# Optimization experiments

Hardware: AMD Instinct MI355X
Metric: run time of the kernel (lower is better)

## Reference

```python
import jax, jax.numpy as jnp
import numpy as np

N_NODES = 50000
N_EDGES = 800000
NFEAT = 256
NHID = 128
NCLASS = 40
NLAYERS = 3


def setup_inputs() -> dict:
    key = jax.random.key(0)
    ks = jax.random.split(key, 8)
    x = jax.random.normal(ks[0], (N_NODES, NFEAT), dtype=jnp.float32)
    edge_src = jax.random.randint(ks[1], (N_EDGES,), 0, N_NODES, dtype=jnp.int32)
    edge_dst = jax.random.randint(ks[2], (N_EDGES,), 0, N_NODES, dtype=jnp.int32)
    # Kaiming-ish scaled params
    W_in = jax.random.normal(ks[3], (NFEAT, NHID), dtype=jnp.float32) / np.sqrt(NFEAT)
    b_in = jnp.zeros((NHID,), dtype=jnp.float32)
    W_mlps = jax.random.normal(ks[4], (NLAYERS, NHID, NHID), dtype=jnp.float32) / np.sqrt(NHID)
    b_mlps = jnp.zeros((NLAYERS, NHID), dtype=jnp.float32)
    W_out = jax.random.normal(ks[5], (NHID, NCLASS), dtype=jnp.float32) / np.sqrt(NHID)
    b_out = jnp.zeros((NCLASS,), dtype=jnp.float32)
    return {"x": x, "edge_src": edge_src, "edge_dst": edge_dst,
            "W_in": W_in, "b_in": b_in, "W_mlps": W_mlps, "b_mlps": b_mlps,
            "W_out": W_out, "b_out": b_out}


def reference(x, edge_src, edge_dst, W_in, b_in, W_mlps, b_mlps, W_out, b_out):
    # Dropout is identity in eval mode (training=False).
    n = x.shape[0]
    h = jax.nn.relu(x @ W_in + b_in)                       # [N, H]
    for i in range(NLAYERS):
        # GINConv with eps=0: h' = h + sum_{(s->d) in E} h[s] scattered to d
        agg = jax.ops.segment_sum(h[edge_src], edge_dst, num_segments=n)
        h = jax.nn.relu((h + agg) @ W_mlps[i] + b_mlps[i])  # [N, H]
    logits = h @ W_out + b_out                              # [N, C]
    return jax.nn.log_softmax(logits, axis=1)
```

## Files before the change

kernel.cpp:

```cpp
#include <hip/hip_runtime.h>
#include <math.h>

#define NHID 128
#define NFEAT 256
#define NCLASS 40

typedef __bf16 bf16x8 __attribute__((ext_vector_type(8)));
typedef __bf16 bf16x4 __attribute__((ext_vector_type(4)));
typedef float floatx4 __attribute__((ext_vector_type(4)));


__global__ __launch_bounds__(256) void bucket_hist(const int* __restrict__ edst,
                                                   int* __restrict__ bucket_counts,
                                                   int E, int nbuck) {
    __shared__ int lh[256];
    int tid = threadIdx.x;
    lh[tid] = 0;
    __syncthreads();
    int base = blockIdx.x * 4096;
#pragma unroll
    for (int k = 0; k < 16; ++k) {
        int e = base + k * 256 + tid;
        if (e < E) atomicAdd(&lh[edst[e] >> 8], 1);
    }
    __syncthreads();
    if (tid < nbuck && lh[tid]) atomicAdd(&bucket_counts[tid], lh[tid]);
}

__global__ __launch_bounds__(256) void bucket_scan(const int* __restrict__ counts,
                                                   int* __restrict__ start,
                                                   int* __restrict__ cursor,
                                                   int* __restrict__ row_ptr,
                                                   int nbuck, int E, int N) {
    __shared__ int lds[256];
    int tid = threadIdx.x;
    int v = (tid < nbuck) ? counts[tid] : 0;
    lds[tid] = v;
    __syncthreads();
    for (int off = 1; off < 256; off <<= 1) {
        int t = (tid >= off) ? lds[tid - off] : 0;
        __syncthreads();
        lds[tid] += t;
        __syncthreads();
    }
    int excl = lds[tid] - v;
    if (tid < nbuck) { start[tid] = excl; cursor[tid] = excl; }
    if (tid == 0) { start[nbuck] = E; row_ptr[N] = E; }
}

__global__ __launch_bounds__(256) void bucket_scatter(const int* __restrict__ esrc,
                                                      const int* __restrict__ edst,
                                                      int* __restrict__ cursor,
                                                      unsigned int* __restrict__ bdata,
                                                      int E, int nbuck) {
    __shared__ int lh[256];
    __shared__ int lbase[256];
    int tid = threadIdx.x;
    lh[tid] = 0;
    __syncthreads();
    int base = blockIdx.x * 4096;
    unsigned int recs[16];
    short bks[16];
    short lofs[16];
#pragma unroll
    for (int k = 0; k < 16; ++k) {
        int e = base + k * 256 + tid;
        bks[k] = -1;
        if (e < E) {
            int d = edst[e];
            int s = esrc[e];
            int b = d >> 8;
            recs[k] = ((unsigned int)(d & 255) << 16) | (unsigned int)s;
            bks[k] = (short)b;
            lofs[k] = (short)atomicAdd(&lh[b], 1);
        }
    }
    __syncthreads();
    if (tid < nbuck && lh[tid]) lbase[tid] = atomicAdd(&cursor[tid], lh[tid]);
    __syncthreads();
#pragma unroll
    for (int k = 0; k < 16; ++k) {
        if (bks[k] >= 0) bdata[lbase[bks[k]] + lofs[k]] = recs[k];
    }
}

__global__ __launch_bounds__(256) void bucket_finalize(const unsigned int* __restrict__ bdata,
                                                       const int* __restrict__ start,
                                                       int* __restrict__ row_ptr,
                                                       int* __restrict__ srcs,
                                                       int N) {
    __shared__ int hist[256];
    __shared__ int cur[256];
    int b = blockIdx.x;
    int tid = threadIdx.x;
    int s0 = start[b];
    int cnt = start[b + 1] - s0;
    hist[tid] = 0;
    __syncthreads();
    for (int i = tid; i < cnt; i += 256) atomicAdd(&hist[bdata[s0 + i] >> 16], 1);
    __syncthreads();
    int v0 = hist[tid];
    __syncthreads();
    for (int off = 1; off < 256; off <<= 1) {
        int t = (tid >= off) ? hist[tid - off] : 0;
        __syncthreads();
        hist[tid] += t;
        __syncthreads();
    }
    int excl = hist[tid] - v0;
    cur[tid] = excl;
    int node = b * 256 + tid;
    if (node < N) row_ptr[node] = s0 + excl;
    __syncthreads();
    for (int i = tid; i < cnt; i += 256) {
        unsigned int r = bdata[s0 + i];
        int p = atomicAdd(&cur[r >> 16], 1);
        srcs[s0 + p] = (int)(r & 0xffffu);
    }
}

__global__ __launch_bounds__(256) void transpose_split_all(
    const float* __restrict__ Win, const float* __restrict__ Wmlps,
    __bf16* __restrict__ dInHi, __bf16* __restrict__ dInLo,
    __bf16* __restrict__ dMlHi, __bf16* __restrict__ dMlLo) {
    const int TOT_IN = 128 * NFEAT;
    const int TOT_ML = 3 * 128 * NHID;
    int i = blockIdx.x * 256 + threadIdx.x;
    if (i < TOT_IN) {
        int n = i / NFEAT;
        int k = i - n * NFEAT;
        float v = Win[(size_t)k * 128 + n];
        __bf16 h = (__bf16)v;
        dInHi[i] = h;
        dInLo[i] = (__bf16)(v - (float)h);
    } else if (i < TOT_IN + TOT_ML) {
        int r = i - TOT_IN;
        int per = 128 * NHID;
        int l = r / per;
        int rr = r - l * per;
        int n = rr / NHID;
        int k = rr - n * NHID;
        float v = Wmlps[(size_t)l * per + (size_t)k * 128 + n];
        __bf16 h = (__bf16)v;
        dMlHi[r] = h;
        dMlLo[r] = (__bf16)(v - (float)h);
    }
}

__global__ __launch_bounds__(256) void aggregate_fused(const __bf16* __restrict__ hhi,
                                                       const __bf16* __restrict__ hlo,
                                                       const int* __restrict__ row_ptr,
                                                       const int* __restrict__ srcs,
                                                       __bf16* __restrict__ ohi,
                                                       __bf16* __restrict__ olo, int N) {
    int tid = threadIdx.x;
    int node = blockIdx.x * 4 + (tid >> 6);
    if (node >= N) return;
    int lane = tid & 63;
    int g = lane >> 4;
    int c = lane & 15;
    int beg = row_ptr[node];
    int end = row_ptr[node + 1];
    const bf16x8* hv = (const bf16x8*)hhi;

    bf16x8 sh = hv[(size_t)node * 16 + c];
    bf16x8 sl = ((const bf16x8*)hlo)[(size_t)node * 16 + c];

    float a[8], b2[8];
#pragma unroll
    for (int j = 0; j < 8; ++j) { a[j] = 0.f; b2[j] = 0.f; }

    int i = beg;
    for (; i + 16 <= end; i += 16) {
        int s0 = __builtin_nontemporal_load(&srcs[i + g]);
        int s1 = __builtin_nontemporal_load(&srcs[i + 4 + g]);
        int s2 = __builtin_nontemporal_load(&srcs[i + 8 + g]);
        int s3 = __builtin_nontemporal_load(&srcs[i + 12 + g]);
        bf16x8 v0 = hv[(size_t)s0 * 16 + c];
        bf16x8 v1 = hv[(size_t)s1 * 16 + c];
        bf16x8 v2 = hv[(size_t)s2 * 16 + c];
        bf16x8 v3 = hv[(size_t)s3 * 16 + c];
#pragma unroll
        for (int j = 0; j < 8; ++j) {
            a[j] += (float)v0[j] + (float)v2[j];
            b2[j] += (float)v1[j] + (float)v3[j];
        }
    }
    for (; i + 8 <= end; i += 8) {
        int s0 = __builtin_nontemporal_load(&srcs[i + g]);
        int s1 = __builtin_nontemporal_load(&srcs[i + 4 + g]);
        bf16x8 v0 = hv[(size_t)s0 * 16 + c];
        bf16x8 v1 = hv[(size_t)s1 * 16 + c];
#pragma unroll
        for (int j = 0; j < 8; ++j) { a[j] += (float)v0[j]; b2[j] += (float)v1[j]; }
    }
    for (; i < end; i += 4) {
        if (i + g < end) {
            int s = __builtin_nontemporal_load(&srcs[i + g]);
            bf16x8 v = hv[(size_t)s * 16 + c];
#pragma unroll
            for (int j = 0; j < 8; ++j) a[j] += (float)v[j];
        }
    }
#pragma unroll
    for (int j = 0; j < 8; ++j) a[j] += b2[j];
#pragma unroll
    for (int j = 0; j < 8; ++j) a[j] += __shfl_xor(a[j], 16);
#pragma unroll
    for (int j = 0; j < 8; ++j) a[j] += __shfl_xor(a[j], 32);

    if (g == 0) {
        bf16x8 whi, wlo;
#pragma unroll
        for (int j = 0; j < 8; ++j) {
            float v = a[j] + (float)sh[j] + (float)sl[j];
            __bf16 h = (__bf16)v;
            whi[j] = h;
            wlo[j] = (__bf16)(v - (float)h);
        }
        ((bf16x8*)ohi)[(size_t)node * 16 + c] = whi;
        ((bf16x8*)olo)[(size_t)node * 16 + c] = wlo;
    }
}

template <int MODE>
__global__ __launch_bounds__(256) void gemm_mfma(
    const float* __restrict__ Af, const __bf16* __restrict__ Ahi,
    const __bf16* __restrict__ Alo,
    const __bf16* __restrict__ Wthi, const __bf16* __restrict__ Wtlo,
    const float* __restrict__ bias, __bf16* __restrict__ Ohi,
    __bf16* __restrict__ Olo, int M, int K) {
    __shared__ __align__(16) char smem[49152];
    __bf16* sAhi = (__bf16*)smem;
    __bf16* sAlo = (__bf16*)(smem + 8192);
    __bf16* sWhi = (__bf16*)(smem + 16384);
    __bf16* sWlo = (__bf16*)(smem + 32768);

    int tid = threadIdx.x;
    int row0 = blockIdx.x * 64;
    int wave = tid >> 6;
    int l = tid & 63;
    int m16 = l & 15;
    int q = l >> 4;
    int axor = m16 & 7;
    int arow = wave * 16 + m16;

    floatx4 acc[8];
#pragma unroll
    for (int t = 0; t < 8; ++t) acc[t] = (floatx4){0.f, 0.f, 0.f, 0.f};

    for (int k0 = 0; k0 < K; k0 += 64) {
#pragma unroll
        for (int it = 0; it < 2; ++it) {
            int lin = it * 2048 + tid * 8;
            int row = lin >> 6, k = lin & 63;
            int g = min(row0 + row, M - 1);
            int off = row * 64 + (((k >> 3) ^ (row & 7)) << 3);
            if (MODE == 0) {
                float4 v0 = *(const float4*)&Af[(size_t)g * K + k0 + k];
                float4 v1 = *(const float4*)&Af[(size_t)g * K + k0 + k + 4];
                float s[8] = {v0.x, v0.y, v0.z, v0.w, v1.x, v1.y, v1.z, v1.w};
                bf16x8 shi, slo;
#pragma unroll
                for (int j = 0; j < 8; ++j) {
                    __bf16 h = (__bf16)s[j];
                    shi[j] = h;
                    slo[j] = (__bf16)(s[j] - (float)h);
                }
                *(bf16x8*)(sAhi + off) = shi;
                *(bf16x8*)(sAlo + off) = slo;
            } else {
                *(bf16x8*)(sAhi + off) = *(const bf16x8*)&Ahi[(size_t)g * 128 + k0 + k];
                *(bf16x8*)(sAlo + off) = *(const bf16x8*)&Alo[(size_t)g * 128 + k0 + k];
            }
        }
#pragma unroll
        for (int it = 0; it < 4; ++it) {
            int lin = it * 2048 + tid * 8;
            int n = lin >> 6, kk = lin & 63;
            int off = n * 64 + (((kk >> 3) ^ (n & 7)) << 3);
            *(bf16x8*)(sWhi + off) = *(const bf16x8*)&Wthi[(size_t)n * K + k0 + kk];
            *(bf16x8*)(sWlo + off) = *(const bf16x8*)&Wtlo[(size_t)n * K + k0 + kk];
        }
        __syncthreads();

#pragma unroll
        for (int s = 0; s < 2; ++s) {
            int sw = (((s * 4 + q) ^ axor) << 3);
            bf16x8 ahi = *(bf16x8*)(sAhi + arow * 64 + sw);
            bf16x8 alo = *(bf16x8*)(sAlo + arow * 64 + sw);
#pragma unroll
            for (int t = 0; t < 8; ++t) {
                int n = t * 16 + m16;
                bf16x8 bhi = *(bf16x8*)(sWhi + n * 64 + sw);
                bf16x8 blo = *(bf16x8*)(sWlo + n * 64 + sw);
                acc[t] = __builtin_amdgcn_mfma_f32_16x16x32_bf16(ahi, bhi, acc[t], 0, 0, 0);
                acc[t] = __builtin_amdgcn_mfma_f32_16x16x32_bf16(alo, bhi, acc[t], 0, 0, 0);
                acc[t] = __builtin_amdgcn_mfma_f32_16x16x32_bf16(ahi, blo, acc[t], 0, 0, 0);
            }
        }
        __syncthreads();
    }

    float* eps = (float*)(smem + 16384);
#pragma unroll
    for (int t = 0; t < 8; ++t) {
        int col = t * 16 + m16;
        float bb = bias[col];
#pragma unroll
        for (int i = 0; i < 4; ++i) {
            int row = wave * 16 + q * 4 + i;
            eps[row * 128 + col] = fmaxf(acc[t][i] + bb, 0.f);
        }
    }
    __syncthreads();
#pragma unroll
    for (int it = 0; it < 8; ++it) {
        int lin = it * 1024 + tid * 4;
        int row = lin >> 7, col = lin & 127;
        int g = row0 + row;
        if (g < M) {
            float4 v = *(float4*)(eps + lin);
            bf16x4 hi, lo;
            float vv[4] = {v.x, v.y, v.z, v.w};
#pragma unroll
            for (int j = 0; j < 4; ++j) {
                __bf16 h = (__bf16)vv[j];
                hi[j] = h;
                lo[j] = (__bf16)(vv[j] - (float)h);
            }
            *(bf16x4*)&Ohi[(size_t)g * 128 + col] = hi;
            *(bf16x4*)&Olo[(size_t)g * 128 + col] = lo;
        }
    }
}

__global__ __launch_bounds__(256) void gemm_out(
    const __bf16* __restrict__ Ahi, const __bf16* __restrict__ Alo,
    const __bf16* __restrict__ Wthi, const __bf16* __restrict__ Wtlo,
    const float* __restrict__ bias,
    const float* __restrict__ Wout, const float* __restrict__ bout,
    float* __restrict__ out, int M) {
    __shared__ __align__(16) char smem[57344];
    __bf16* sAhi = (__bf16*)smem;
    __bf16* sAlo = (__bf16*)(smem + 8192);
    __bf16* sWhi = (__bf16*)(smem + 16384);
    __bf16* sWlo = (__bf16*)(smem + 32768);

    int tid = threadIdx.x;
    int row0 = blockIdx.x * 64;
    int wave = tid >> 6;
    int l = tid & 63;
    int m16 = l & 15;
    int q = l >> 4;
    int axor = m16 & 7;
    int arow = wave * 16 + m16;

    floatx4 acc[8];
#pragma unroll
    for (int t = 0; t < 8; ++t) acc[t] = (floatx4){0.f, 0.f, 0.f, 0.f};

    for (int k0 = 0; k0 < 128; k0 += 64) {
#pragma unroll
        for (int it = 0; it < 2; ++it) {
            int lin = it * 2048 + tid * 8;
            int row = lin >> 6, k = lin & 63;
            int g = min(row0 + row, M - 1);
            int off = row * 64 + (((k >> 3) ^ (row & 7)) << 3);
            *(bf16x8*)(sAhi + off) = *(const bf16x8*)&Ahi[(size_t)g * 128 + k0 + k];
            *(bf16x8*)(sAlo + off) = *(const bf16x8*)&Alo[(size_t)g * 128 + k0 + k];
        }
#pragma unroll
        for (int it = 0; it < 4; ++it) {
            int lin = it * 2048 + tid * 8;
            int n = lin >> 6, kk = lin & 63;
            int off = n * 64 + (((kk >> 3) ^ (n & 7)) << 3);
            *(bf16x8*)(sWhi + off) = *(const bf16x8*)&Wthi[(size_t)n * 128 + k0 + kk];
            *(bf16x8*)(sWlo + off) = *(const bf16x8*)&Wtlo[(size_t)n * 128 + k0 + kk];
        }
        __syncthreads();

#pragma unroll
        for (int s = 0; s < 2; ++s) {
            int sw = (((s * 4 + q) ^ axor) << 3);
            bf16x8 ahi = *(bf16x8*)(sAhi + arow * 64 + sw);
            bf16x8 alo = *(bf16x8*)(sAlo + arow * 64 + sw);
#pragma unroll
            for (int t = 0; t < 8; ++t) {
                int n = t * 16 + m16;
                bf16x8 bhi = *(bf16x8*)(sWhi + n * 64 + sw);
                bf16x8 blo = *(bf16x8*)(sWlo + n * 64 + sw);
                acc[t] = __builtin_amdgcn_mfma_f32_16x16x32_bf16(ahi, bhi, acc[t], 0, 0, 0);
                acc[t] = __builtin_amdgcn_mfma_f32_16x16x32_bf16(alo, bhi, acc[t], 0, 0, 0);
                acc[t] = __builtin_amdgcn_mfma_f32_16x16x32_bf16(ahi, blo, acc[t], 0, 0, 0);
            }
        }
        __syncthreads();
    }

    float* eps = (float*)smem;
    float* sWo = (float*)(smem + 34816);
    float* sb  = (float*)(smem + 55296);
#pragma unroll
    for (int t = 0; t < 8; ++t) {
        int col = t * 16 + m16;
        float bb = bias[col];
#pragma unroll
        for (int i = 0; i < 4; ++i) {
            int row = wave * 16 + q * 4 + i;
            eps[row * 132 + col] = fmaxf(acc[t][i] + bb, 0.f);
        }
    }
    for (int i = tid; i < 128 * NCLASS; i += 256) sWo[i] = Wout[i];
    if (tid < NCLASS) sb[tid] = bout[tid];
    __syncthreads();

    int r = tid >> 2;
    int cg = tid & 3;
    float z[10];
#pragma unroll
    for (int j = 0; j < 10; ++j) z[j] = sb[cg * 10 + j];
    for (int k = 0; k < 128; ++k) {
        float a = eps[r * 132 + k];
#pragma unroll
        for (int j = 0; j < 10; ++j) z[j] += a * sWo[k * NCLASS + cg * 10 + j];
    }
    float m = z[0];
#pragma unroll
    for (int j = 1; j < 10; ++j) m = fmaxf(m, z[j]);
    m = fmaxf(m, __shfl_xor(m, 1));
    m = fmaxf(m, __shfl_xor(m, 2));
    float s = 0.f;
#pragma unroll
    for (int j = 0; j < 10; ++j) s += expf(z[j] - m);
    s += __shfl_xor(s, 1);
    s += __shfl_xor(s, 2);
    float lse = m + logf(s);
    int row = row0 + r;
    if (row < M) {
#pragma unroll
        for (int j = 0; j < 10; ++j) out[(size_t)row * NCLASS + cg * 10 + j] = z[j] - lse;
    }
}

extern "C" void kernel_launch(void* const* d_in, const int* in_sizes, int n_in,
                              void* d_out, int out_size, void* d_ws, size_t ws_size,
                              hipStream_t stream) {
    const float* x      = (const float*)d_in[0];
    const int*   esrc   = (const int*)d_in[1];
    const int*   edst   = (const int*)d_in[2];
    const float* W_in   = (const float*)d_in[3];
    const float* b_in   = (const float*)d_in[4];
    const float* W_mlps = (const float*)d_in[5];
    const float* b_mlps = (const float*)d_in[6];
    const float* W_out  = (const float*)d_in[7];
    const float* b_out  = (const float*)d_in[8];
    float* out = (float*)d_out;

    int N = in_sizes[0] / NFEAT;
    int E = in_sizes[1];
    int nbuck = (N + 255) >> 8;

    char* ws = (char*)d_ws;
    size_t hb = (((size_t)N * NHID * sizeof(__bf16)) + 255) & ~(size_t)255;
    __bf16* h_hi_a = (__bf16*)ws;
    __bf16* h_lo_a = (__bf16*)(ws + hb);
    __bf16* h_hi_b = (__bf16*)(ws + 2 * hb);
    __bf16* h_lo_b = (__bf16*)(ws + 3 * hb);
    __bf16* sum_hi = (__bf16*)(ws + 4 * hb);
    __bf16* sum_lo = (__bf16*)(ws + 5 * hb);
    unsigned int* bdata = (unsigned int*)(ws + 4 * hb);
    char* ip = ws + 6 * hb;
    int* row_ptr = (int*)ip;  ip += (((size_t)(N + 1) * 4) + 255) & ~(size_t)255;
    int* srcs    = (int*)ip;  ip += (((size_t)E * 4) + 255) & ~(size_t)255;
    int* bucket_counts = (int*)ip;  ip += 1024;
    int* bucket_start  = (int*)ip;  ip += 1024;
    int* bucket_cursor = (int*)ip;  ip += 1024;
    __bf16* Wt_in_hi   = (__bf16*)ip;  ip += 128 * NFEAT * 2;
    __bf16* Wt_in_lo   = (__bf16*)ip;  ip += 128 * NFEAT * 2;
    __bf16* Wt_mlps_hi = (__bf16*)ip;  ip += 3 * 128 * NHID * 2;
    __bf16* Wt_mlps_lo = (__bf16*)ip;  ip += 3 * 128 * NHID * 2;

    int eb4 = (E + 4095) / 4096;

    hipMemsetAsync(bucket_counts, 0, 1024, stream);
    bucket_hist<<<eb4, 256, 0, stream>>>(edst, bucket_counts, E, nbuck);
    bucket_scan<<<1, 256, 0, stream>>>(bucket_counts, bucket_start, bucket_cursor,
                                       row_ptr, nbuck, E, N);
    bucket_scatter<<<eb4, 256, 0, stream>>>(esrc, edst, bucket_cursor, bdata, E, nbuck);
    bucket_finalize<<<nbuck, 256, 0, stream>>>(bdata, bucket_start, row_ptr, srcs, N);

    transpose_split_all<<<(128 * NFEAT + 3 * 128 * NHID + 255) / 256, 256, 0, stream>>>(
        W_in, W_mlps, Wt_in_hi, Wt_in_lo, Wt_mlps_hi, Wt_mlps_lo);

    int gb = (N + 63) / 64;
    gemm_mfma<0><<<gb, 256, 0, stream>>>(x, (const __bf16*)nullptr, (const __bf16*)nullptr,
                                         Wt_in_hi, Wt_in_lo, b_in, h_hi_a, h_lo_a, N, NFEAT);

    __bf16* cur_hi = h_hi_a; __bf16* cur_lo = h_lo_a;
    __bf16* nxt_hi = h_hi_b; __bf16* nxt_lo = h_lo_b;
    for (int i = 0; i < 2; ++i) {
        aggregate_fused<<<(N + 3) / 4, 256, 0, stream>>>(cur_hi, cur_lo, row_ptr, srcs,
                                                         sum_hi, sum_lo, N);
        gemm_mfma<1><<<gb, 256, 0, stream>>>(
            (const float*)nullptr, sum_hi, sum_lo,
            Wt_mlps_hi + (size_t)i * 128 * NHID, Wt_mlps_lo + (size_t)i * 128 * NHID,
            b_mlps + (size_t)i * NHID, nxt_hi, nxt_lo, N, NHID);
        __bf16* t;
        t = cur_hi; cur_hi = nxt_hi; nxt_hi = t;
        t = cur_lo; cur_lo = nxt_lo; nxt_lo = t;
    }

    aggregate_fused<<<(N + 3) / 4, 256, 0, stream>>>(cur_hi, cur_lo, row_ptr, srcs,
                                                     sum_hi, sum_lo, N);
    gemm_out<<<gb, 256, 0, stream>>>(sum_hi, sum_lo,
                                     Wt_mlps_hi + (size_t)2 * 128 * NHID,
                                     Wt_mlps_lo + (size_t)2 * 128 * NHID,
                                     b_mlps + (size_t)2 * NHID,
                                     W_out, b_out, out, N);
}
```

Before: 324.1 us.

## Merge graph-preprocessing launches and fuse CSR finalize with input GEMM

Cuts the launch sequence from memset, hist, scan, scatter, finalize, transpose and gemm down to three kernels. Histogram, weight transpose and cursor init now share one launch. The scatter and finalize kernels each recompute the bucket prefix sum from per-block partial histograms, which removes the separate scan kernel. The CSR finalize runs in the same grid as the input GEMM, with one block range per role, so the two overlap. The cost is redundant per-block summing of eb4×256 partial counts, and the input GEMM now depends on scatter finishing.

```diff
diff --git a/kernel.cpp b/kernel.cpp
--- a/kernel.cpp
+++ b/kernel.cpp
@@ -1,5 +1,6 @@
 #include <hip/hip_runtime.h>
 #include <math.h>
+
 
 #define NHID 128
 #define NFEAT 256
@@ -10,54 +11,193 @@
 typedef float floatx4 __attribute__((ext_vector_type(4)));
 
 
-__global__ __launch_bounds__(256) void bucket_hist(const int* __restrict__ edst,
-                                                   int* __restrict__ bucket_counts,
-                                                   int E, int nbuck) {
-    __shared__ int lh[256];
+__device__ __forceinline__ void scan256(int* sbuf, int tid) {
+    for (int off = 1; off < 256; off <<= 1) {
+        int tmp = (tid >= off) ? sbuf[tid - off] : 0;
+        __syncthreads();
+        sbuf[tid] += tmp;
+        __syncthreads();
+    }
+}
+
+template <int MODE>
+__device__ __forceinline__ void gemm_body(
+    char* smem, const float* __restrict__ Af, const __bf16* __restrict__ Ahi,
+    const __bf16* __restrict__ Alo,
+    const __bf16* __restrict__ Wthi, const __bf16* __restrict__ Wtlo,
+    const float* __restrict__ bias, __bf16* __restrict__ Ohi,
+    __bf16* __restrict__ Olo, int M, int K, int row0, int tid) {
+    __bf16* sAhi = (__bf16*)smem;
+    __bf16* sAlo = (__bf16*)(smem + 8192);
+    __bf16* sWhi = (__bf16*)(smem + 16384);
+    __bf16* sWlo = (__bf16*)(smem + 32768);
+
+    int wave = tid >> 6;
+    int l = tid & 63;
+    int m16 = l & 15;
+    int q = l >> 4;
+    int axor = m16 & 7;
+    int arow = wave * 16 + m16;
+
+    floatx4 acc[8];
+#pragma unroll
+    for (int t = 0; t < 8; ++t) acc[t] = (floatx4){0.f, 0.f, 0.f, 0.f};
+
+    for (int k0 = 0; k0 < K; k0 += 64) {
+#pragma unroll
+        for (int it = 0; it < 2; ++it) {
+            int lin = it * 2048 + tid * 8;
+            int row = lin >> 6, k = lin & 63;
+            int g = min(row0 + row, M - 1);
+            int off = row * 64 + (((k >> 3) ^ (row & 7)) << 3);
+            if (MODE == 0) {
+                float4 v0 = *(const float4*)&Af[(size_t)g * K + k0 + k];
+                float4 v1 = *(const float4*)&Af[(size_t)g * K + k0 + k + 4];
+                float s[8] = {v0.x, v0.y, v0.z, v0.w, v1.x, v1.y, v1.z, v1.w};
+                bf16x8 shi, slo;
+#pragma unroll
+                for (int j = 0; j < 8; ++j) {
+                    __bf16 h = (__bf16)s[j];
+                    shi[j] = h;
+                    slo[j] = (__bf16)(s[j] - (float)h);
+                }
+                *(bf16x8*)(sAhi + off) = shi;
+                *(bf16x8*)(sAlo + off) = slo;
+            } else {
+                *(bf16x8*)(sAhi + off) = *(const bf16x8*)&Ahi[(size_t)g * 128 + k0 + k];
+                *(bf16x8*)(sAlo + off) = *(const bf16x8*)&Alo[(size_t)g * 128 + k0 + k];
+            }
+        }
+#pragma unroll
+        for (int it = 0; it < 4; ++it) {
+            int lin = it * 2048 + tid * 8;
+            int n = lin >> 6, kk = lin & 63;
+            int off = n * 64 + (((kk >> 3) ^ (n & 7)) << 3);
+            *(bf16x8*)(sWhi + off) = *(const bf16x8*)&Wthi[(size_t)n * K + k0 + kk];
+            *(bf16x8*)(sWlo + off) = *(const bf16x8*)&Wtlo[(size_t)n * K + k0 + kk];
+        }
+        __syncthreads();
+
+#pragma unroll
+        for (int s = 0; s < 2; ++s) {
+            int sw = (((s * 4 + q) ^ axor) << 3);
+            bf16x8 ahi = *(bf16x8*)(sAhi + arow * 64 + sw);
+            bf16x8 alo = *(bf16x8*)(sAlo + arow * 64 + sw);
+#pragma unroll
+            for (int t = 0; t < 8; ++t) {
+                int n = t * 16 + m16;
+                bf16x8 bhi = *(bf16x8*)(sWhi + n * 64 + sw);
+                bf16x8 blo = *(bf16x8*)(sWlo + n * 64 + sw);
+                acc[t] = __builtin_amdgcn_mfma_f32_16x16x32_bf16(ahi, bhi, acc[t], 0, 0, 0);
+                acc[t] = __builtin_amdgcn_mfma_f32_16x16x32_bf16(alo, bhi, acc[t], 0, 0, 0);
+                acc[t] = __builtin_amdgcn_mfma_f32_16x16x32_bf16(ahi, blo, acc[t], 0, 0, 0);
+            }
+        }
+        __syncthreads();
+    }
+
+    float* eps = (float*)(smem + 16384);
+#pragma unroll
+    for (int t = 0; t < 8; ++t) {
+        int col = t * 16 + m16;
+        float bb = bias[col];
+#pragma unroll
+        for (int i = 0; i < 4; ++i) {
+            int row = wave * 16 + q * 4 + i;
+            eps[row * 128 + col] = fmaxf(acc[t][i] + bb, 0.f);
+        }
+    }
+    __syncthreads();
+#pragma unroll
+    for (int it = 0; it < 8; ++it) {
+        int lin = it * 1024 + tid * 4;
+        int row = lin >> 7, col = lin & 127;
+        int g = row0 + row;
+        if (g < M) {
+            float4 v = *(float4*)(eps + lin);
+            bf16x4 hi, lo;
+            float vv[4] = {v.x, v.y, v.z, v.w};
+#pragma unroll
+            for (int j = 0; j < 4; ++j) {
+                __bf16 h = (__bf16)vv[j];
+                hi[j] = h;
+                lo[j] = (__bf16)(vv[j] - (float)h);
+            }
+            *(bf16x4*)&Ohi[(size_t)g * 128 + col] = hi;
+            *(bf16x4*)&Olo[(size_t)g * 128 + col] = lo;
+        }
+    }
+}
+
+__global__ __launch_bounds__(256) void prep(
+    const int* __restrict__ edst, int* __restrict__ phist, int E, int eb4,
+    const float* __restrict__ Win, const float* __restrict__ Wmlps,
+    __bf16* __restrict__ dInHi, __bf16* __restrict__ dInLo,
+    __bf16* __restrict__ dMlHi, __bf16* __restrict__ dMlLo,
+    int* __restrict__ cursor, int* __restrict__ row_ptr, int N) {
+    __shared__ int lhist[256];
     int tid = threadIdx.x;
-    lh[tid] = 0;
-    __syncthreads();
-    int base = blockIdx.x * 4096;
-#pragma unroll
-    for (int k = 0; k < 16; ++k) {
-        int e = base + k * 256 + tid;
-        if (e < E) atomicAdd(&lh[edst[e] >> 8], 1);
-    }
-    __syncthreads();
-    if (tid < nbuck && lh[tid]) atomicAdd(&bucket_counts[tid], lh[tid]);
-}
-
-__global__ __launch_bounds__(256) void bucket_scan(const int* __restrict__ counts,
-                                                   int* __restrict__ start,
-                                                   int* __restrict__ cursor,
-                                                   int* __restrict__ row_ptr,
-                                                   int nbuck, int E, int N) {
-    __shared__ int lds[256];
-    int tid = threadIdx.x;
-    int v = (tid < nbuck) ? counts[tid] : 0;
-    lds[tid] = v;
-    __syncthreads();
-    for (int off = 1; off < 256; off <<= 1) {
-        int t = (tid >= off) ? lds[tid - off] : 0;
-        __syncthreads();
-        lds[tid] += t;
-        __syncthreads();
-    }
-    int excl = lds[tid] - v;
-    if (tid < nbuck) { start[tid] = excl; cursor[tid] = excl; }
-    if (tid == 0) { start[nbuck] = E; row_ptr[N] = E; }
-}
-
-__global__ __launch_bounds__(256) void bucket_scatter(const int* __restrict__ esrc,
-                                                      const int* __restrict__ edst,
-                                                      int* __restrict__ cursor,
-                                                      unsigned int* __restrict__ bdata,
-                                                      int E, int nbuck) {
-    __shared__ int lh[256];
+    int bid = blockIdx.x;
+    if (bid < eb4) {
+        lhist[tid] = 0;
+        __syncthreads();
+        int base = bid * 4096;
+#pragma unroll
+        for (int k = 0; k < 16; ++k) {
+            int e = base + k * 256 + tid;
+            if (e < E) atomicAdd(&lhist[edst[e] >> 8], 1);
+        }
+        __syncthreads();
+        phist[bid * 256 + tid] = lhist[tid];
+    } else if (bid < eb4 + 320) {
+        const int TOT_IN = 128 * NFEAT;
+        const int TOT_ML = 3 * 128 * NHID;
+        int i = (bid - eb4) * 256 + tid;
+        if (i < TOT_IN) {
+            int n = i / NFEAT;
+            int k = i - n * NFEAT;
+            float v = Win[(size_t)k * 128 + n];
+            __bf16 h = (__bf16)v;
+            dInHi[i] = h;
+            dInLo[i] = (__bf16)(v - (float)h);
+        } else if (i < TOT_IN + TOT_ML) {
+            int r = i - TOT_IN;
+            int per = 128 * NHID;
+            int l = r / per;
+            int rr = r - l * per;
+            int n = rr / NHID;
+            int k = rr - n * NHID;
+            float v = Wmlps[(size_t)l * per + (size_t)k * 128 + n];
+            __bf16 h = (__bf16)v;
+            dMlHi[r] = h;
+            dMlLo[r] = (__bf16)(v - (float)h);
+        }
+    } else {
+        cursor[tid] = 0;
+        if (tid == 0) row_ptr[N] = E;
+    }
+}
+
+__global__ __launch_bounds__(256) void scatter(const int* __restrict__ esrc,
+                                               const int* __restrict__ edst,
+                                               const int* __restrict__ phist,
+                                               int* __restrict__ cursor,
+                                               unsigned int* __restrict__ bdata,
+                                               int E, int eb4) {
+    __shared__ int sscan[256];
+    __shared__ int sstart[256];
+    __shared__ int lhist[256];
     __shared__ int lbase[256];
     int tid = threadIdx.x;
-    lh[tid] = 0;
+    int tot = 0;
+    for (int p = 0; p < eb4; ++p) tot += phist[p * 256 + tid];
+    sscan[tid] = tot;
     __syncthreads();
+    scan256(sscan, tid);
+    sstart[tid] = sscan[tid] - tot;
+    lhist[tid] = 0;
+    __syncthreads();
+
     int base = blockIdx.x * 4096;
     unsigned int recs[16];
     short bks[16];
@@ -72,11 +212,11 @@
             int b = d >> 8;
             recs[k] = ((unsigned int)(d & 255) << 16) | (unsigned int)s;
             bks[k] = (short)b;
-            lofs[k] = (short)atomicAdd(&lh[b], 1);
+            lofs[k] = (short)atomicAdd(&lhist[b], 1);
         }
     }
     __syncthreads();
-    if (tid < nbuck && lh[tid]) lbase[tid] = atomicAdd(&cursor[tid], lh[tid]);
+    if (lhist[tid]) lbase[tid] = sstart[tid] + atomicAdd(&cursor[tid], lhist[tid]);
     __syncthreads();
 #pragma unroll
     for (int k = 0; k < 16; ++k) {
@@ -84,66 +224,49 @@
     }
 }
 
-__global__ __launch_bounds__(256) void bucket_finalize(const unsigned int* __restrict__ bdata,
-                                                       const int* __restrict__ start,
-                                                       int* __restrict__ row_ptr,
-                                                       int* __restrict__ srcs,
-                                                       int N) {
-    __shared__ int hist[256];
-    __shared__ int cur[256];
-    int b = blockIdx.x;
+__global__ __launch_bounds__(256) void fin_gemmin(
+    const unsigned int* __restrict__ bdata, const int* __restrict__ phist,
+    int eb4, int nbuck, int* __restrict__ row_ptr, int* __restrict__ srcs, int N,
+    const float* __restrict__ Af,
+    const __bf16* __restrict__ Wthi, const __bf16* __restrict__ Wtlo,
+    const float* __restrict__ bias, __bf16* __restrict__ Ohi,
+    __bf16* __restrict__ Olo) {
+    __shared__ __align__(16) char smem[49152];
     int tid = threadIdx.x;
-    int s0 = start[b];
-    int cnt = start[b + 1] - s0;
-    hist[tid] = 0;
-    __syncthreads();
-    for (int i = tid; i < cnt; i += 256) atomicAdd(&hist[bdata[s0 + i] >> 16], 1);
-    __syncthreads();
-    int v0 = hist[tid];
-    __syncthreads();
-    for (int off = 1; off < 256; off <<= 1) {
-        int t = (tid >= off) ? hist[tid - off] : 0;
-        __syncthreads();
-        hist[tid] += t;
-        __syncthreads();
-    }
-    int excl = hist[tid] - v0;
-    cur[tid] = excl;
-    int node = b * 256 + tid;
-    if (node < N) row_ptr[node] = s0 + excl;
-    __syncthreads();
-    for (int i = tid; i < cnt; i += 256) {
-        unsigned int r = bdata[s0 + i];
-        int p = atomicAdd(&cur[r >> 16], 1);
-        srcs[s0 + p] = (int)(r & 0xffffu);
-    }
-}
-
-__global__ __launch_bounds__(256) void transpose_split_all(
-    const float* __restrict__ Win, const float* __restrict__ Wmlps,
-    __bf16* __restrict__ dInHi, __bf16* __restrict__ dInLo,
-    __bf16* __restrict__ dMlHi, __bf16* __restrict__ dMlLo) {
-    const int TOT_IN = 128 * NFEAT;
-    const int TOT_ML = 3 * 128 * NHID;
-    int i = blockIdx.x * 256 + threadIdx.x;
-    if (i < TOT_IN) {
-        int n = i / NFEAT;
-        int k = i - n * NFEAT;
-        float v = Win[(size_t)k * 128 + n];
-        __bf16 h = (__bf16)v;
-        dInHi[i] = h;
-        dInLo[i] = (__bf16)(v - (float)h);
-    } else if (i < TOT_IN + TOT_ML) {
-        int r = i - TOT_IN;
-        int per = 128 * NHID;
-        int l = r / per;
-        int rr = r - l * per;
-        int n = rr / NHID;
-        int k = rr - n * NHID;
-        float v = Wmlps[(size_t)l * per + (size_t)k * 128 + n];
-        __bf16 h = (__bf16)v;
-        dMlHi[r] = h;
-        dMlLo[r] = (__bf16)(v - (float)h);
+    if ((int)blockIdx.x < nbuck) {
+        int* sscan = (int*)smem;
+        int* nhist = (int*)(smem + 1024);
+        int* wcur  = (int*)(smem + 2048);
+        int b = blockIdx.x;
+        int tot = 0;
+        for (int p = 0; p < eb4; ++p) tot += phist[p * 256 + tid];
+        sscan[tid] = tot;
+        __syncthreads();
+        scan256(sscan, tid);
+        int s0 = (b > 0) ? sscan[b - 1] : 0;
+        int cnt = sscan[b] - s0;
+        __syncthreads();
+        nhist[tid] = 0;
+        __syncthreads();
+        for (int i = tid; i < cnt; i += 256) atomicAdd(&nhist[bdata[s0 + i] >> 16], 1);
+        __syncthreads();
+        int v0 = nhist[tid];
+        __syncthreads();
+        scan256(nhist, tid);
+        int excl = nhist[tid] - v0;
+        wcur[tid] = excl;
+        int node = b * 256 + tid;
+        if (node < N) row_ptr[node] = s0 + excl;
+        __syncthreads();
+        for (int i = tid; i < cnt; i += 256) {
+            unsigned int r = bdata[s0 + i];
+            int p = atomicAdd(&wcur[r >> 16], 1);
+            srcs[s0 + p] = (int)(r & 0xffffu);
+        }
+    } else {
+        int row0 = ((int)blockIdx.x - nbuck) * 64;
+        gemm_body<0>(smem, Af, (const __bf16*)nullptr, (const __bf16*)nullptr,
+                     Wthi, Wtlo, bias, Ohi, Olo, N, NFEAT, row0, tid);
     }
 }
 
@@ -163,8 +286,8 @@
     int end = row_ptr[node + 1];
     const bf16x8* hv = (const bf16x8*)hhi;
 
-    bf16x8 sh = hv[(size_t)node * 16 + c];
-    bf16x8 sl = ((const bf16x8*)hlo)[(size_t)node * 16 + c];
+    bf16x8 selfhi = hv[(size_t)node * 16 + c];
+    bf16x8 selflo = ((const bf16x8*)hlo)[(size_t)node * 16 + c];
 
     float a[8], b2[8];
 #pragma unroll
@@ -213,7 +336,7 @@
         bf16x8 whi, wlo;
 #pragma unroll
         for (int j = 0; j < 8; ++j) {
-            float v = a[j] + (float)sh[j] + (float)sl[j];
+            float v = a[j] + (float)selfhi[j] + (float)selflo[j];
             __bf16 h = (__bf16)v;
             whi[j] = h;
             wlo[j] = (__bf16)(v - (float)h);
@@ -223,116 +346,14 @@
     }
 }
 
-template <int MODE>
-__global__ __launch_bounds__(256) void gemm_mfma(
-    const float* __restrict__ Af, const __bf16* __restrict__ Ahi,
-    const __bf16* __restrict__ Alo,
+__global__ __launch_bounds__(256) void gemm_layer(
+    const __bf16* __restrict__ Ahi, const __bf16* __restrict__ Alo,
     const __bf16* __restrict__ Wthi, const __bf16* __restrict__ Wtlo,
     const float* __restrict__ bias, __bf16* __restrict__ Ohi,
-    __bf16* __restrict__ Olo, int M, int K) {
+    __bf16* __restrict__ Olo, int M) {
     __shared__ __align__(16) char smem[49152];
-    __bf16* sAhi = (__bf16*)smem;
-    __bf16* sAlo = (__bf16*)(smem + 8192);
-    __bf16* sWhi = (__bf16*)(smem + 16384);
-    __bf16* sWlo = (__bf16*)(smem + 32768);
-
-    int tid = threadIdx.x;
-    int row0 = blockIdx.x * 64;
-    int wave = tid >> 6;
-    int l = tid & 63;
-    int m16 = l & 15;
-    int q = l >> 4;
-    int axor = m16 & 7;
-    int arow = wave * 16 + m16;
-
-    floatx4 acc[8];
-#pragma unroll
-    for (int t = 0; t < 8; ++t) acc[t] = (floatx4){0.f, 0.f, 0.f, 0.f};
-
-    for (int k0 = 0; k0 < K; k0 += 64) {
-#pragma unroll
-        for (int it = 0; it < 2; ++it) {
-            int lin = it * 2048 + tid * 8;
-            int row = lin >> 6, k = lin & 63;
-            int g = min(row0 + row, M - 1);
-            int off = row * 64 + (((k >> 3) ^ (row & 7)) << 3);
-            if (MODE == 0) {
-                float4 v0 = *(const float4*)&Af[(size_t)g * K + k0 + k];
-                float4 v1 = *(const float4*)&Af[(size_t)g * K + k0 + k + 4];
-                float s[8] = {v0.x, v0.y, v0.z, v0.w, v1.x, v1.y, v1.z, v1.w};
-                bf16x8 shi, slo;
-#pragma unroll
-                for (int j = 0; j < 8; ++j) {
-                    __bf16 h = (__bf16)s[j];
-                    shi[j] = h;
-                    slo[j] = (__bf16)(s[j] - (float)h);
-                }
-                *(bf16x8*)(sAhi + off) = shi;
-                *(bf16x8*)(sAlo + off) = slo;
-            } else {
-                *(bf16x8*)(sAhi + off) = *(const bf16x8*)&Ahi[(size_t)g * 128 + k0 + k];
-                *(bf16x8*)(sAlo + off) = *(const bf16x8*)&Alo[(size_t)g * 128 + k0 + k];
-            }
-        }
-#pragma unroll
-        for (int it = 0; it < 4; ++it) {
-            int lin = it * 2048 + tid * 8;
-            int n = lin >> 6, kk = lin & 63;
-            int off = n * 64 + (((kk >> 3) ^ (n & 7)) << 3);
-            *(bf16x8*)(sWhi + off) = *(const bf16x8*)&Wthi[(size_t)n * K + k0 + kk];
-            *(bf16x8*)(sWlo + off) = *(const bf16x8*)&Wtlo[(size_t)n * K + k0 + kk];
-        }
-        __syncthreads();
-
-#pragma unroll
-        for (int s = 0; s < 2; ++s) {
-            int sw = (((s * 4 + q) ^ axor) << 3);
-            bf16x8 ahi = *(bf16x8*)(sAhi + arow * 64 + sw);
-            bf16x8 alo = *(bf16x8*)(sAlo + arow * 64 + sw);
-#pragma unroll
-            for (int t = 0; t < 8; ++t) {
-                int n = t * 16 + m16;
-                bf16x8 bhi = *(bf16x8*)(sWhi + n * 64 + sw);
-                bf16x8 blo = *(bf16x8*)(sWlo + n * 64 + sw);
-                acc[t] = __builtin_amdgcn_mfma_f32_16x16x32_bf16(ahi, bhi, acc[t], 0, 0, 0);
-                acc[t] = __builtin_amdgcn_mfma_f32_16x16x32_bf16(alo, bhi, acc[t], 0, 0, 0);
-                acc[t] = __builtin_amdgcn_mfma_f32_16x16x32_bf16(ahi, blo, acc[t], 0, 0, 0);
-            }
-        }
-        __syncthreads();
-    }
-
-    float* eps = (float*)(smem + 16384);
-#pragma unroll
-    for (int t = 0; t < 8; ++t) {
-        int col = t * 16 + m16;
-        float bb = bias[col];
-#pragma unroll
-        for (int i = 0; i < 4; ++i) {
-            int row = wave * 16 + q * 4 + i;
-            eps[row * 128 + col] = fmaxf(acc[t][i] + bb, 0.f);
-        }
-    }
-    __syncthreads();
-#pragma unroll
-    for (int it = 0; it < 8; ++it) {
-        int lin = it * 1024 + tid * 4;
-        int row = lin >> 7, col = lin & 127;
-        int g = row0 + row;
-        if (g < M) {
-            float4 v = *(float4*)(eps + lin);
-            bf16x4 hi, lo;
-            float vv[4] = {v.x, v.y, v.z, v.w};
-#pragma unroll
-            for (int j = 0; j < 4; ++j) {
-                __bf16 h = (__bf16)vv[j];
-                hi[j] = h;
-                lo[j] = (__bf16)(vv[j] - (float)h);
-            }
-            *(bf16x4*)&Ohi[(size_t)g * 128 + col] = hi;
-            *(bf16x4*)&Olo[(size_t)g * 128 + col] = lo;
-        }
-    }
+    gemm_body<1>(smem, (const float*)nullptr, Ahi, Alo, Wthi, Wtlo, bias,
+                 Ohi, Olo, M, NHID, blockIdx.x * 64, threadIdx.x);
 }
 
 __global__ __launch_bounds__(256) void gemm_out(
@@ -460,6 +481,7 @@
     int N = in_sizes[0] / NFEAT;
     int E = in_sizes[1];
     int nbuck = (N + 255) >> 8;
+    int eb4 = (E + 4095) / 4096;
 
     char* ws = (char*)d_ws;
     size_t hb = (((size_t)N * NHID * sizeof(__bf16)) + 255) & ~(size_t)255;
@@ -473,39 +495,31 @@
     char* ip = ws + 6 * hb;
     int* row_ptr = (int*)ip;  ip += (((size_t)(N + 1) * 4) + 255) & ~(size_t)255;
     int* srcs    = (int*)ip;  ip += (((size_t)E * 4) + 255) & ~(size_t)255;
-    int* bucket_counts = (int*)ip;  ip += 1024;
-    int* bucket_start  = (int*)ip;  ip += 1024;
-    int* bucket_cursor = (int*)ip;  ip += 1024;
+    int* phist   = (int*)ip;  ip += (size_t)eb4 * 256 * 4;
+    int* cursor  = (int*)ip;  ip += 1024;
     __bf16* Wt_in_hi   = (__bf16*)ip;  ip += 128 * NFEAT * 2;
     __bf16* Wt_in_lo   = (__bf16*)ip;  ip += 128 * NFEAT * 2;
     __bf16* Wt_mlps_hi = (__bf16*)ip;  ip += 3 * 128 * NHID * 2;
     __bf16* Wt_mlps_lo = (__bf16*)ip;  ip += 3 * 128 * NHID * 2;
 
-    int eb4 = (E + 4095) / 4096;
-
-    hipMemsetAsync(bucket_counts, 0, 1024, stream);
-    bucket_hist<<<eb4, 256, 0, stream>>>(edst, bucket_counts, E, nbuck);
-    bucket_scan<<<1, 256, 0, stream>>>(bucket_counts, bucket_start, bucket_cursor,
-                                       row_ptr, nbuck, E, N);
-    bucket_scatter<<<eb4, 256, 0, stream>>>(esrc, edst, bucket_cursor, bdata, E, nbuck);
-    bucket_finalize<<<nbuck, 256, 0, stream>>>(bdata, bucket_start, row_ptr, srcs, N);
-
-    transpose_split_all<<<(128 * NFEAT + 3 * 128 * NHID + 255) / 256, 256, 0, stream>>>(
-        W_in, W_mlps, Wt_in_hi, Wt_in_lo, Wt_mlps_hi, Wt_mlps_lo);
-
     int gb = (N + 63) / 64;
-    gemm_mfma<0><<<gb, 256, 0, stream>>>(x, (const __bf16*)nullptr, (const __bf16*)nullptr,
-                                         Wt_in_hi, Wt_in_lo, b_in, h_hi_a, h_lo_a, N, NFEAT);
+
+    prep<<<eb4 + 320 + 1, 256, 0, stream>>>(edst, phist, E, eb4, W_in, W_mlps,
+                                            Wt_in_hi, Wt_in_lo, Wt_mlps_hi, Wt_mlps_lo,
+                                            cursor, row_ptr, N);
+    scatter<<<eb4, 256, 0, stream>>>(esrc, edst, phist, cursor, bdata, E, eb4);
+    fin_gemmin<<<nbuck + gb, 256, 0, stream>>>(bdata, phist, eb4, nbuck, row_ptr, srcs, N,
+                                               x, Wt_in_hi, Wt_in_lo, b_in, h_hi_a, h_lo_a);
 
     __bf16* cur_hi = h_hi_a; __bf16* cur_lo = h_lo_a;
     __bf16* nxt_hi = h_hi_b; __bf16* nxt_lo = h_lo_b;
     for (int i = 0; i < 2; ++i) {
         aggregate_fused<<<(N + 3) / 4, 256, 0, stream>>>(cur_hi, cur_lo, row_ptr, srcs,
                                                          sum_hi, sum_lo, N);
-        gemm_mfma<1><<<gb, 256, 0, stream>>>(
-            (const float*)nullptr, sum_hi, sum_lo,
+        gemm_layer<<<gb, 256, 0, stream>>>(
+            sum_hi, sum_lo,
             Wt_mlps_hi + (size_t)i * 128 * NHID, Wt_mlps_lo + (size_t)i * 128 * NHID,
-            b_mlps + (size_t)i * NHID, nxt_hi, nxt_lo, N, NHID);
+            b_mlps + (size_t)i * NHID, nxt_hi, nxt_lo, N);
         __bf16* t;
         t = cur_hi; cur_hi = nxt_hi; nxt_hi = t;
         t = cur_lo; cur_lo = nxt_lo; nxt_lo = t;
```

After: 347.6 us. 1.07x slower.

## Load GEMM operands directly from global memory into MFMA registers, drop LDS staging

Applied to the files above, without the earlier changes.

The hidden-layer and output GEMMs no longer stage A and W tiles through shared memory. Each lane now loads its MFMA fragments straight from global memory, which relies on L1/L2 caching for the weights shared across blocks, and K becomes a template parameter so the loop fully unrolls. The epilogue writes results through a smaller shared buffer in two 32-row halves, which cuts LDS use to raise occupancy and removes the per-K-step barriers. The trade-off is that weight fragments are re-read from cache by every wave instead of once per block, and each row's global loads are strided and narrower.

```diff
diff --git a/kernel.cpp b/kernel.cpp
--- a/kernel.cpp
+++ b/kernel.cpp
@@ -223,223 +223,180 @@
     }
 }
 
-template <int MODE>
-__global__ __launch_bounds__(256) void gemm_mfma(
+template <int MODE, int K>
+__global__ __launch_bounds__(256) void gemm_direct(
     const float* __restrict__ Af, const __bf16* __restrict__ Ahi,
     const __bf16* __restrict__ Alo,
     const __bf16* __restrict__ Wthi, const __bf16* __restrict__ Wtlo,
     const float* __restrict__ bias, __bf16* __restrict__ Ohi,
-    __bf16* __restrict__ Olo, int M, int K) {
-    __shared__ __align__(16) char smem[49152];
-    __bf16* sAhi = (__bf16*)smem;
-    __bf16* sAlo = (__bf16*)(smem + 8192);
-    __bf16* sWhi = (__bf16*)(smem + 16384);
-    __bf16* sWlo = (__bf16*)(smem + 32768);
-
+    __bf16* __restrict__ Olo, int M) {
+    __shared__ __align__(16) float eps[32 * 128];
     int tid = threadIdx.x;
     int row0 = blockIdx.x * 64;
     int wave = tid >> 6;
     int l = tid & 63;
     int m16 = l & 15;
     int q = l >> 4;
-    int axor = m16 & 7;
-    int arow = wave * 16 + m16;
+    int garow = min(row0 + wave * 16 + m16, M - 1);
 
     floatx4 acc[8];
 #pragma unroll
     for (int t = 0; t < 8; ++t) acc[t] = (floatx4){0.f, 0.f, 0.f, 0.f};
 
+#pragma unroll
     for (int k0 = 0; k0 < K; k0 += 64) {
 #pragma unroll
-        for (int it = 0; it < 2; ++it) {
-            int lin = it * 2048 + tid * 8;
-            int row = lin >> 6, k = lin & 63;
-            int g = min(row0 + row, M - 1);
-            int off = row * 64 + (((k >> 3) ^ (row & 7)) << 3);
+        for (int s = 0; s < 2; ++s) {
+            int kk = k0 + s * 32 + q * 8;
+            bf16x8 ahi, alo;
             if (MODE == 0) {
-                float4 v0 = *(const float4*)&Af[(size_t)g * K + k0 + k];
-                float4 v1 = *(const float4*)&Af[(size_t)g * K + k0 + k + 4];
-                float s[8] = {v0.x, v0.y, v0.z, v0.w, v1.x, v1.y, v1.z, v1.w};
-                bf16x8 shi, slo;
+                float4 v0 = *(const float4*)&Af[(size_t)garow * K + kk];
+                float4 v1 = *(const float4*)&Af[(size_t)garow * K + kk + 4];
+                float sv[8] = {v0.x, v0.y, v0.z, v0.w, v1.x, v1.y, v1.z, v1.w};
 #pragma unroll
                 for (int j = 0; j < 8; ++j) {
-                    __bf16 h = (__bf16)s[j];
-                    shi[j] = h;
-                    slo[j] = (__bf16)(s[j] - (float)h);
+                    __bf16 h = (__bf16)sv[j];
+                    ahi[j] = h;
+                    alo[j] = (__bf16)(sv[j] - (float)h);
                 }
-                *(bf16x8*)(sAhi + off) = shi;
-                *(bf16x8*)(sAlo + off) = slo;
             } else {
-                *(bf16x8*)(sAhi + off) = *(const bf16x8*)&Ahi[(size_t)g * 128 + k0 + k];
-                *(bf16x8*)(sAlo + off) = *(const bf16x8*)&Alo[(size_t)g * 128 + k0 + k];
-            }
-        }
-#pragma unroll
-        for (int it = 0; it < 4; ++it) {
-            int lin = it * 2048 + tid * 8;
-            int n = lin >> 6, kk = lin & 63;
-            int off = n * 64 + (((kk >> 3) ^ (n & 7)) << 3);
-            *(bf16x8*)(sWhi + off) = *(const bf16x8*)&Wthi[(size_t)n * K + k0 + kk];
-            *(bf16x8*)(sWlo + off) = *(const bf16x8*)&Wtlo[(size_t)n * K + k0 + kk];
-        }
-        __syncthreads();
-
-#pragma unroll
-        for (int s = 0; s < 2; ++s) {
-            int sw = (((s * 4 + q) ^ axor) << 3);
-            bf16x8 ahi = *(bf16x8*)(sAhi + arow * 64 + sw);
-            bf16x8 alo = *(bf16x8*)(sAlo + arow * 64 + sw);
+                ahi = *(const bf16x8*)&Ahi[(size_t)garow * K + kk];
+                alo = *(const bf16x8*)&Alo[(size_t)garow * K + kk];
+            }
 #pragma unroll
             for (int t = 0; t < 8; ++t) {
                 int n = t * 16 + m16;
-                bf16x8 bhi = *(bf16x8*)(sWhi + n * 64 + sw);
-                bf16x8 blo = *(bf16x8*)(sWlo + n * 64 + sw);
+                bf16x8 bhi = *(const bf16x8*)&Wthi[(size_t)n * K + kk];
+                bf16x8 blo = *(const bf16x8*)&Wtlo[(size_t)n * K + kk];
                 acc[t] = __builtin_amdgcn_mfma_f32_16x16x32_bf16(ahi, bhi, acc[t], 0, 0, 0);
                 acc[t] = __builtin_amdgcn_mfma_f32_16x16x32_bf16(alo, bhi, acc[t], 0, 0, 0);
                 acc[t] = __builtin_amdgcn_mfma_f32_16x16x32_bf16(ahi, blo, acc[t], 0, 0, 0);
             }
         }
-        __syncthreads();
-    }
-
-    float* eps = (float*)(smem + 16384);
-#pragma unroll
-    for (int t = 0; t < 8; ++t) {
-        int col = t * 16 + m16;
-        float bb = bias[col];
-#pragma unroll
-        for (int i = 0; i < 4; ++i) {
-            int row = wave * 16 + q * 4 + i;
-            eps[row * 128 + col] = fmaxf(acc[t][i] + bb, 0.f);
-        }
-    }
-    __syncthreads();
-#pragma unroll
-    for (int it = 0; it < 8; ++it) {
-        int lin = it * 1024 + tid * 4;
-        int row = lin >> 7, col = lin & 127;
-        int g = row0 + row;
-        if (g < M) {
-            float4 v = *(float4*)(eps + lin);
-            bf16x4 hi, lo;
-            float vv[4] = {v.x, v.y, v.z, v.w};
-#pragma unroll
-            for (int j = 0; j < 4; ++j) {
-                __bf16 h = (__bf16)vv[j];
-                hi[j] = h;
-                lo[j] = (__bf16)(vv[j] - (float)h);
-            }
-            *(bf16x4*)&Ohi[(size_t)g * 128 + col] = hi;
-            *(bf16x4*)&Olo[(size_t)g * 128 + col] = lo;
-        }
-    }
-}
-
-__global__ __launch_bounds__(256) void gemm_out(
+    }
+
+#pragma unroll
+    for (int half = 0; half < 2; ++half) {
+        if ((wave >> 1) == half) {
+#pragma unroll
+            for (int t = 0; t < 8; ++t) {
+                int col = t * 16 + m16;
+                float bb = bias[col];
+#pragma unroll
+                for (int i = 0; i < 4; ++i) {
+                    int lr = (wave & 1) * 16 + q * 4 + i;
+                    eps[lr * 128 + col] = fmaxf(acc[t][i] + bb, 0.f);
+                }
+            }
+        }
+        __syncthreads();
+#pragma unroll
+        for (int it = 0; it < 4; ++it) {
+            int lin = it * 1024 + tid * 4;
+            int row = lin >> 7, col = lin & 127;
+            int g = row0 + half * 32 + row;
+            if (g < M) {
+                float4 v = *(float4*)(eps + lin);
+                bf16x4 hi, lo;
+                float vv[4] = {v.x, v.y, v.z, v.w};
+#pragma unroll
+                for (int j = 0; j < 4; ++j) {
+                    __bf16 h = (__bf16)vv[j];
+                    hi[j] = h;
+                    lo[j] = (__bf16)(vv[j] - (float)h);
+                }
+                *(bf16x4*)&Ohi[(size_t)g * 128 + col] = hi;
+                *(bf16x4*)&Olo[(size_t)g * 128 + col] = lo;
+            }
+        }
+        __syncthreads();
+    }
+}
+
+__global__ __launch_bounds__(256) void gemm_out_direct(
     const __bf16* __restrict__ Ahi, const __bf16* __restrict__ Alo,
     const __bf16* __restrict__ Wthi, const __bf16* __restrict__ Wtlo,
     const float* __restrict__ bias,
     const float* __restrict__ Wout, const float* __restrict__ bout,
     float* __restrict__ out, int M) {
-    __shared__ __align__(16) char smem[57344];
-    __bf16* sAhi = (__bf16*)smem;
-    __bf16* sAlo = (__bf16*)(smem + 8192);
-    __bf16* sWhi = (__bf16*)(smem + 16384);
-    __bf16* sWlo = (__bf16*)(smem + 32768);
-
+    __shared__ __align__(16) char smem[37664];
+    float* eps = (float*)smem;
+    float* sWo = (float*)(smem + 16896);
+    float* sb  = (float*)(smem + 37376);
     int tid = threadIdx.x;
     int row0 = blockIdx.x * 64;
     int wave = tid >> 6;
     int l = tid & 63;
     int m16 = l & 15;
     int q = l >> 4;
-    int axor = m16 & 7;
-    int arow = wave * 16 + m16;
+    int garow = min(row0 + wave * 16 + m16, M - 1);
 
     floatx4 acc[8];
 #pragma unroll
     for (int t = 0; t < 8; ++t) acc[t] = (floatx4){0.f, 0.f, 0.f, 0.f};
 
+#pragma unroll
     for (int k0 = 0; k0 < 128; k0 += 64) {
 #pragma unroll
-        for (int it = 0; it < 2; ++it) {
-            int lin = it * 2048 + tid * 8;
-            int row = lin >> 6, k = lin & 63;
-            int g = min(row0 + row, M - 1);
-            int off = row * 64 + (((k >> 3) ^ (row & 7)) << 3);
-            *(bf16x8*)(sAhi + off) = *(const bf16x8*)&Ahi[(size_t)g * 128 + k0 + k];
-            *(bf16x8*)(sAlo + off) = *(const bf16x8*)&Alo[(size_t)g * 128 + k0 + k];
-        }
-#pragma unroll
-        for (int it = 0; it < 4; ++it) {
-            int lin = it * 2048 + tid * 8;
-            int n = lin >> 6, kk = lin & 63;
-            int off = n * 64 + (((kk >> 3) ^ (n & 7)) << 3);
-            *(bf16x8*)(sWhi + off) = *(const bf16x8*)&Wthi[(size_t)n * 128 + k0 + kk];
-            *(bf16x8*)(sWlo + off) = *(const bf16x8*)&Wtlo[(size_t)n * 128 + k0 + kk];
-        }
-        __syncthreads();
-
-#pragma unroll
         for (int s = 0; s < 2; ++s) {
-            int sw = (((s * 4 + q) ^ axor) << 3);
-            bf16x8 ahi = *(bf16x8*)(sAhi + arow * 64 + sw);
-            bf16x8 alo = *(bf16x8*)(sAlo + arow * 64 + sw);
+            int kk = k0 + s * 32 + q * 8;
+            bf16x8 ahi = *(const bf16x8*)&Ahi[(size_t)garow * 128 + kk];
+            bf16x8 alo = *(const bf16x8*)&Alo[(size_t)garow * 128 + kk];
 #pragma unroll
             for (int t = 0; t < 8; ++t) {
                 int n = t * 16 + m16;
-                bf16x8 bhi = *(bf16x8*)(sWhi + n * 64 + sw);
-                bf16x8 blo = *(bf16x8*)(sWlo + n * 64 + sw);
+                bf16x8 bhi = *(const bf16x8*)&Wthi[(size_t)n * 128 + kk];
+                bf16x8 blo = *(const bf16x8*)&Wtlo[(size_t)n * 128 + kk];
                 acc[t] = __builtin_amdgcn_mfma_f32_16x16x32_bf16(ahi, bhi, acc[t], 0, 0, 0);
                 acc[t] = __builtin_amdgcn_mfma_f32_16x16x32_bf16(alo, bhi, acc[t], 0, 0, 0);
                 acc[t] = __builtin_amdgcn_mfma_f32_16x16x32_bf16(ahi, blo, acc[t], 0, 0, 0);
             }
         }
-        __syncthreads();
-    }
-
-    float* eps = (float*)smem;
-    float* sWo = (float*)(smem + 34816);
-    float* sb  = (float*)(smem + 55296);
-#pragma unroll
-    for (int t = 0; t < 8; ++t) {
-        int col = t * 16 + m16;
-        float bb = bias[col];
-#pragma unroll
-        for (int i = 0; i < 4; ++i) {
-            int row = wave * 16 + q * 4 + i;
-            eps[row * 132 + col] = fmaxf(acc[t][i] + bb, 0.f);
-        }
-    }
+    }
+
     for (int i = tid; i < 128 * NCLASS; i += 256) sWo[i] = Wout[i];
     if (tid < NCLASS) sb[tid] = bout[tid];
-    __syncthreads();
-
-    int r = tid >> 2;
-    int cg = tid & 3;
-    float z[10];
-#pragma unroll
-    for (int j = 0; j < 10; ++j) z[j] = sb[cg * 10 + j];
-    for (int k = 0; k < 128; ++k) {
-        float a = eps[r * 132 + k];
-#pragma unroll
-        for (int j = 0; j < 10; ++j) z[j] += a * sWo[k * NCLASS + cg * 10 + j];
-    }
-    float m = z[0];
-#pragma unroll
-    for (int j = 1; j < 10; ++j) m = fmaxf(m, z[j]);
-    m = fmaxf(m, __shfl_xor(m, 1));
-    m = fmaxf(m, __shfl_xor(m, 2));
-    float s = 0.f;
-#pragma unroll
-    for (int j = 0; j < 10; ++j) s += expf(z[j] - m);
-    s += __shfl_xor(s, 1);
-    s += __shfl_xor(s, 2);
-    float lse = m + logf(s);
-    int row = row0 + r;
-    if (row < M) {
-#pragma unroll
-        for (int j = 0; j < 10; ++j) out[(size_t)row * NCLASS + cg * 10 + j] = z[j] - lse;
+
+#pragma unroll
+    for (int half = 0; half < 2; ++half) {
+        if ((wave >> 1) == half) {
+#pragma unroll
+            for (int t = 0; t < 8; ++t) {
+                int col = t * 16 + m16;
+                float bb = bias[col];
+#pragma unroll
+                for (int i = 0; i < 4; ++i) {
+                    int lr = (wave & 1) * 16 + q * 4 + i;
+                    eps[lr * 132 + col] = fmaxf(acc[t][i] + bb, 0.f);
+                }
+            }
+        }
+        __syncthreads();
+        int r = tid >> 3;
+        int cg = tid & 7;
+        float z[5];
+#pragma unroll
+        for (int j = 0; j < 5; ++j) z[j] = sb[cg * 5 + j];
+        for (int k = 0; k < 128; ++k) {
+            float a = eps[r * 132 + k];
+#pragma unroll
+            for (int j = 0; j < 5; ++j) z[j] += a * sWo[k * NCLASS + cg * 5 + j];
+        }
+        float m = z[0];
+#pragma unroll
+        for (int j = 1; j < 5; ++j) m = fmaxf(m, z[j]);
+        for (int off = 1; off < 8; off <<= 1) m = fmaxf(m, __shfl_xor(m, off));
+        float s = 0.f;
+#pragma unroll
+        for (int j = 0; j < 5; ++j) s += expf(z[j] - m);
+        for (int off = 1; off < 8; off <<= 1) s += __shfl_xor(s, off);
+        float lse = m + logf(s);
+        int row = row0 + half * 32 + r;
+        if (row < M) {
+#pragma unroll
+            for (int j = 0; j < 5; ++j) out[(size_t)row * NCLASS + cg * 5 + j] = z[j] - lse;
+        }
+        __syncthreads();
     }
 }
 
@@ -494,18 +451,19 @@
         W_in, W_mlps, Wt_in_hi, Wt_in_lo, Wt_mlps_hi, Wt_mlps_lo);
 
     int gb = (N + 63) / 64;
-    gemm_mfma<0><<<gb, 256, 0, stream>>>(x, (const __bf16*)nullptr, (const __bf16*)nullptr,
-                                         Wt_in_hi, Wt_in_lo, b_in, h_hi_a, h_lo_a, N, NFEAT);
+    gemm_direct<0, NFEAT><<<gb, 256, 0, stream>>>(
+        x, (const __bf16*)nullptr, (const __bf16*)nullptr,
+        Wt_in_hi, Wt_in_lo, b_in, h_hi_a, h_lo_a, N);
 
     __bf16* cur_hi = h_hi_a; __bf16* cur_lo = h_lo_a;
     __bf16* nxt_hi = h_hi_b; __bf16* nxt_lo = h_lo_b;
     for (int i = 0; i < 2; ++i) {
         aggregate_fused<<<(N + 3) / 4, 256, 0, stream>>>(cur_hi, cur_lo, row_ptr, srcs,
                                                          sum_hi, sum_lo, N);
-        gemm_mfma<1><<<gb, 256, 0, stream>>>(
+        gemm_direct<1, NHID><<<gb, 256, 0, stream>>>(
             (const float*)nullptr, sum_hi, sum_lo,
             Wt_mlps_hi + (size_t)i * 128 * NHID, Wt_mlps_lo + (size_t)i * 128 * NHID,
-            b_mlps + (size_t)i * NHID, nxt_hi, nxt_lo, N, NHID);
+            b_mlps + (size_t)i * NHID, nxt_hi, nxt_lo, N);
         __bf16* t;
         t = cur_hi; cur_hi = nxt_hi; nxt_hi = t;
         t = cur_lo; cur_lo = nxt_lo; nxt_lo = t;
@@ -513,9 +471,9 @@
 
     aggregate_fused<<<(N + 3) / 4, 256, 0, stream>>>(cur_hi, cur_lo, row_ptr, srcs,
                                                      sum_hi, sum_lo, N);
-    gemm_out<<<gb, 256, 0, stream>>>(sum_hi, sum_lo,
-                                     Wt_mlps_hi + (size_t)2 * 128 * NHID,
-                                     Wt_mlps_lo + (size_t)2 * 128 * NHID,
-                                     b_mlps + (size_t)2 * NHID,
-                                     W_out, b_out, out, N);
-}
+    gemm_out_direct<<<gb, 256, 0, stream>>>(sum_hi, sum_lo,
+                                            Wt_mlps_hi + (size_t)2 * 128 * NHID,
+                                            Wt_mlps_lo + (size_t)2 * 128 * NHID,
+                                            b_mlps + (size_t)2 * NHID,
+                                            W_out, b_out, out, N);
+}
```

New measurement: 434.0 us. +33.9%, slower.
